# Performance work log

Hardware: AMD Instinct MI355X
Metric: run time of the kernel (lower is better)

The kernel has to match this reference:

```python
import jax, jax.numpy as jnp
import numpy as np

B, D = 128, 64  # batch; channel == height == width == dim == 64 (hardcoded by the module)


def setup_inputs() -> dict:
    key = jax.random.key(0)
    kx, kc, kh, kw = jax.random.split(key, 4)
    x = jax.random.normal(kx, (B, D, D, D), dtype=jnp.float32)
    # Stacked 1x1 conv weights: [i (loop index), out_channels, in_channels]
    Wc = jax.random.normal(kc, (D, D, D), dtype=jnp.float32) * 0.1
    Wh = jax.random.normal(kh, (D, D, D), dtype=jnp.float32) * 0.1
    Ww = jax.random.normal(kw, (D, D, D), dtype=jnp.float32) * 0.1
    return {"x": x, "Wc": Wc, "Wh": Wh, "Ww": Ww}


def reference(x, Wc, Wh, Ww):
    # x: [b, c, h, w] with c == h == w == 64
    # Adaptive avg-pool to 1x1 on three permutations -> three [b, 64] vectors.
    c_vec = x.mean(axis=(2, 3))  # pool over (h, w): channel descriptor   [b, 64]
    h_vec = x.mean(axis=(1, 2))  # pool over (c, h): width descriptor    [b, 64]
    w_vec = x.mean(axis=(1, 3))  # pool over (c, w): height descriptor   [b, 64]

    # All 64 per-iteration 1x1 convs + sigmoid as one batched GEMM per branch.
    # Wc[i, o, j]: weight of the i-th conv; conv(C)[o] = sum_j Wc[i,o,j] * c_vec[b,j]
    fc = jax.nn.sigmoid(jnp.einsum('ioj,bj->bio', Wc, c_vec))  # [b, 64(i), 64]
    fh = jax.nn.sigmoid(jnp.einsum('ioj,bj->bio', Wh, h_vec))  # [b, 64(i), 64]
    fw = jax.nn.sigmoid(jnp.einsum('ioj,bj->bio', Ww, w_vec))  # [b, 64(i), 64]

    # recon: bmm(bmm(C, H), W) == outer product fc_i (x) fh_i (x) fw_i, summed over i.
    LR = jnp.einsum('bic,bip,biq->bcpq', fc, fh, fw)  # [b, 64, 64, 64]
    return LR
```

## Files before the change

kernel.cpp:

```cpp
#include <hip/hip_runtime.h>
#include <hip/hip_bf16.h>


#define NB 128

typedef __attribute__((ext_vector_type(8))) short bf16x8;
typedef __attribute__((ext_vector_type(4))) float f32x4;

__device__ __forceinline__ float bf2f(short s) {
    return __uint_as_float(((unsigned)(unsigned short)s) << 16);
}
__device__ __forceinline__ unsigned packbf2(float a, float b) {
    unsigned ua = __float_as_uint(a); ua += 0x7fffu + ((ua >> 16) & 1u);
    unsigned ub = __float_as_uint(b); ub += 0x7fffu + ((ub >> 16) & 1u);
    return (ua >> 16) | (ub & 0xffff0000u);
}
__device__ __forceinline__ unsigned short f2bf(float f) {
    unsigned u = __float_as_uint(f); u += 0x7fffu + ((u >> 16) & 1u);
    return (unsigned short)(u >> 16);
}

__global__ __launch_bounds__(256) void pool_kernel(const float* __restrict__ x,
                                                   float* __restrict__ cvecT,
                                                   float* __restrict__ hv_part,
                                                   float* __restrict__ wv_part)
{
    const int blk  = blockIdx.x;
    const int b    = blk >> 3;
    const int cblk = blk & 7;
    const int t    = threadIdx.x;
    const int wv   = t >> 6;
    const int l    = t & 63;
    const int lg   = l >> 4;
    const int lw   = l & 15;

    __shared__ float cpart[8][4];
    __shared__ float hsum_l[64];
    __shared__ float wpart[4][64];

    const float* xb = x + (size_t)b * 262144 + (size_t)cblk * 32768;

    float cs[8];
    float acc_h[4] = {0.f, 0.f, 0.f, 0.f};
    float acc_w[4] = {0.f, 0.f, 0.f, 0.f};

#pragma unroll
    for (int cc = 0; cc < 8; ++cc) {
        const float* xc = xb + cc * 4096 + wv * 1024 + 4 * l;
        float sc = 0.f;
#pragma unroll
        for (int k = 0; k < 4; ++k) {
            float4 v = *reinterpret_cast<const float4*>(xc + k * 256);
            float s = (v.x + v.y) + (v.z + v.w);
            sc += s;
            acc_h[k] += s;
            acc_w[0] += v.x; acc_w[1] += v.y; acc_w[2] += v.z; acc_w[3] += v.w;
        }
        cs[cc] = sc;
    }

#pragma unroll
    for (int cc = 0; cc < 8; ++cc) {
        float v = cs[cc];
#pragma unroll
        for (int off = 32; off >= 1; off >>= 1) v += __shfl_xor(v, off, 64);
        if (l == 0) cpart[cc][wv] = v;
    }
#pragma unroll
    for (int k = 0; k < 4; ++k) {
        float v = acc_h[k];
        v += __shfl_xor(v, 1, 64);
        v += __shfl_xor(v, 2, 64);
        v += __shfl_xor(v, 4, 64);
        v += __shfl_xor(v, 8, 64);
        if (lw == 0) hsum_l[wv * 16 + k * 4 + lg] = v;
    }
#pragma unroll
    for (int m = 0; m < 4; ++m) {
        float v = acc_w[m];
        v += __shfl_xor(v, 16, 64);
        v += __shfl_xor(v, 32, 64);
        if (lg == 0) wpart[wv][lw * 4 + m] = v;
    }
    __syncthreads();

    const float scale = 1.f / 4096.f;
    if (t < 8) {
        float s = cpart[t][0] + cpart[t][1] + cpart[t][2] + cpart[t][3];
        cvecT[(cblk * 8 + t) * NB + b] = s * scale;
    }
    if (t < 64) {
        wv_part[(cblk * 64 + t) * NB + b] = hsum_l[t] * scale;
        float ws_ = wpart[0][t] + wpart[1][t] + wpart[2][t] + wpart[3][t];
        hv_part[(cblk * 64 + t) * NB + b] = ws_ * scale;
    }
}

__global__ __launch_bounds__(256) void fvec_kernel(const float* __restrict__ Wc,
                                                   const float* __restrict__ Wh,
                                                   const float* __restrict__ Ww,
                                                   const float* __restrict__ cvecT,
                                                   const float* __restrict__ hv_part,
                                                   const float* __restrict__ wv_part,
                                                   unsigned short* __restrict__ fcT,
                                                   unsigned short* __restrict__ fhT,
                                                   unsigned short* __restrict__ fwT)
{
    const int br = blockIdx.x >> 6;
    const int i  = blockIdx.x & 63;
    const float* W = (br == 0) ? Wc : (br == 1) ? Wh : Ww;
    const float* V = (br == 0) ? cvecT : (br == 1) ? hv_part : wv_part;
    unsigned short* outT = (br == 0) ? fcT : (br == 1) ? fhT : fwT;

    __shared__ float Wt[64][64];
    __shared__ float vl[64 * NB];

    const int t = threadIdx.x;
    {
        const float* Wi = W + (size_t)i * 4096;
#pragma unroll
        for (int r = 0; r < 4; ++r) {
            int f = t + 256 * r;
            float4 v = reinterpret_cast<const float4*>(Wi)[f];
            int o = (4 * f) >> 6;
            int j = (4 * f) & 63;
            Wt[j + 0][o] = v.x; Wt[j + 1][o] = v.y; Wt[j + 2][o] = v.z; Wt[j + 3][o] = v.w;
        }
    }
#pragma unroll
    for (int r = 0; r < 8; ++r) {
        int f = t + 256 * r;
        float4 v = reinterpret_cast<const float4*>(V)[f];
        if (br != 0) {
#pragma unroll
            for (int k = 1; k < 8; ++k) {
                float4 u = reinterpret_cast<const float4*>(V + 8192 * k)[f];
                v.x += u.x; v.y += u.y; v.z += u.z; v.w += u.w;
            }
        }
        reinterpret_cast<float4*>(vl)[f] = v;
    }
    __syncthreads();

    const int og = t & 7;
    const int bg = t >> 3;
    const int o0 = og * 8;
    const int b0 = bg * 4;

    float acc[4][8];
#pragma unroll
    for (int bb = 0; bb < 4; ++bb)
#pragma unroll
        for (int oo = 0; oo < 8; ++oo) acc[bb][oo] = 0.f;

#pragma unroll 4
    for (int j = 0; j < 64; ++j) {
        float4 vb = *reinterpret_cast<const float4*>(&vl[j * NB + b0]);
        float4 w0 = *reinterpret_cast<const float4*>(&Wt[j][o0]);
        float4 w1 = *reinterpret_cast<const float4*>(&Wt[j][o0 + 4]);
        float vb_[4] = {vb.x, vb.y, vb.z, vb.w};
        float wv_[8] = {w0.x, w0.y, w0.z, w0.w, w1.x, w1.y, w1.z, w1.w};
#pragma unroll
        for (int bb = 0; bb < 4; ++bb)
#pragma unroll
            for (int oo = 0; oo < 8; ++oo)
                acc[bb][oo] += vb_[bb] * wv_[oo];
    }

#pragma unroll
    for (int bb = 0; bb < 4; ++bb)
#pragma unroll
        for (int oo = 0; oo < 8; ++oo) {
            float sg = 1.f / (1.f + __expf(-acc[bb][oo]));
            outT[((size_t)(b0 + bb) * 64 + (o0 + oo)) * 64 + i] = f2bf(sg);
        }
}

__global__ __launch_bounds__(256) void recon_kernel(const unsigned short* __restrict__ fcT,
                                                    const unsigned short* __restrict__ fhT,
                                                    const unsigned short* __restrict__ fwT,
                                                    float* __restrict__ out)
{
    const int blk = blockIdx.x;
    const int b   = blk >> 2;
    const int cq  = blk & 3;
    const int t   = threadIdx.x;
    const int w   = t >> 6;
    const int l   = t & 63;
    const int lr  = l & 15;
    const int lg4 = l >> 4;

    __shared__ __align__(16) unsigned short fhl[64 * 72];
    __shared__ __align__(16) unsigned short fwl[64 * 72];
    __shared__ __align__(16) unsigned short fcl[16 * 72];

    const unsigned short* fhb = fhT + (size_t)b * 4096;
    const unsigned short* fwb = fwT + (size_t)b * 4096;
    const unsigned short* fcb = fcT + (size_t)b * 4096 + cq * 1024;

#pragma unroll
    for (int r = 0; r < 2; ++r) {
        int f = t + 256 * r;
        *reinterpret_cast<int4*>(&fhl[(f >> 3) * 72 + (f & 7) * 8]) =
            reinterpret_cast<const int4*>(fhb)[f];
        *reinterpret_cast<int4*>(&fwl[(f >> 3) * 72 + (f & 7) * 8]) =
            reinterpret_cast<const int4*>(fwb)[f];
    }
    if (t < 128) {
        *reinterpret_cast<int4*>(&fcl[(t >> 3) * 72 + (t & 7) * 8]) =
            reinterpret_cast<const int4*>(fcb)[t];
    }
    __syncthreads();

    bf16x8 afw[4][2];
#pragma unroll
    for (int qt = 0; qt < 4; ++qt)
#pragma unroll
        for (int kb = 0; kb < 2; ++kb)
            afw[qt][kb] = *reinterpret_cast<const bf16x8*>(
                &fwl[(qt * 16 + lr) * 72 + kb * 32 + lg4 * 8]);

    float hvf[4][2][8];
#pragma unroll
    for (int pt = 0; pt < 4; ++pt)
#pragma unroll
        for (int kb = 0; kb < 2; ++kb) {
            bf16x8 h = *reinterpret_cast<const bf16x8*>(
                &fhl[(pt * 16 + lr) * 72 + kb * 32 + lg4 * 8]);
#pragma unroll
            for (int j = 0; j < 8; ++j) hvf[pt][kb][j] = bf2f(h[j]);
        }

    for (int cc = 0; cc < 4; ++cc) {
        const int cl = w * 4 + cc;
        float cvf[16];
#pragma unroll
        for (int kb = 0; kb < 2; ++kb) {
            bf16x8 cf = *reinterpret_cast<const bf16x8*>(
                &fcl[cl * 72 + kb * 32 + lg4 * 8]);
#pragma unroll
            for (int j = 0; j < 8; ++j) cvf[kb * 8 + j] = bf2f(cf[j]);
        }
        bf16x8 bp[4][2];
#pragma unroll
        for (int pt = 0; pt < 4; ++pt)
#pragma unroll
            for (int kb = 0; kb < 2; ++kb) {
                union { unsigned u[4]; bf16x8 v; } bu;
#pragma unroll
                for (int jj = 0; jj < 4; ++jj) {
                    float p0 = cvf[kb * 8 + 2 * jj]     * hvf[pt][kb][2 * jj];
                    float p1 = cvf[kb * 8 + 2 * jj + 1] * hvf[pt][kb][2 * jj + 1];
                    bu.u[jj] = packbf2(p0, p1);
                }
                bp[pt][kb] = bu.v;
            }
        float* oc = out + (((size_t)b * 64 + cq * 16 + cl) * 64) * 64;
#pragma unroll
        for (int pt = 0; pt < 4; ++pt)
#pragma unroll
            for (int qt = 0; qt < 4; ++qt) {
                f32x4 a = {0.f, 0.f, 0.f, 0.f};
                a = __builtin_amdgcn_mfma_f32_16x16x32_bf16(afw[qt][0], bp[pt][0], a, 0, 0, 0);
                a = __builtin_amdgcn_mfma_f32_16x16x32_bf16(afw[qt][1], bp[pt][1], a, 0, 0, 0);
                float4 v; v.x = a[0]; v.y = a[1]; v.z = a[2]; v.w = a[3];
                *reinterpret_cast<float4*>(
                    oc + ((size_t)(pt * 16 + lr) * 64) + qt * 16 + lg4 * 4) = v;
            }
    }
}

extern "C" void kernel_launch(void* const* d_in, const int* in_sizes, int n_in,
                              void* d_out, int out_size, void* d_ws, size_t ws_size,
                              hipStream_t stream) {
    (void)in_sizes; (void)n_in; (void)out_size; (void)ws_size;
    const float* x  = (const float*)d_in[0];
    const float* Wc = (const float*)d_in[1];
    const float* Wh = (const float*)d_in[2];
    const float* Ww = (const float*)d_in[3];
    float* out = (float*)d_out;

    float* ws      = (float*)d_ws;
    float* cvecT   = ws;
    float* hv_part = ws + 8192;
    float* wv_part = ws + 73728;
    unsigned short* fcT = (unsigned short*)(ws + 139264);
    unsigned short* fhT = fcT + 524288;
    unsigned short* fwT = fhT + 524288;

    pool_kernel<<<1024, 256, 0, stream>>>(x, cvecT, hv_part, wv_part);
    fvec_kernel<<<192, 256, 0, stream>>>(Wc, Wh, Ww, cvecT, hv_part, wv_part, fcT, fhT, fwT);
    recon_kernel<<<512, 256, 0, stream>>>(fcT, fhT, fwT, out);
}
```

Baseline: 70.98 us.

## Fuse pool, fvec and recon kernels into one persistent kernel with grid barriers

Merges the three launches into a single 512-block kernel that uses atomic-counter grid barriers between the pooling, gate-GEMM and reconstruction phases. This removes two kernel launch gaps. The pool phase now covers 16 channels per block, so there are 4 partial slices instead of 8 to sum. It relies on all 512 blocks being co-resident (launch_bounds 256,2 and 48KB of shared memory), adds a memset launch, and risks deadlock or barrier spin overhead if occupancy is insufficient.

```diff
diff --git a/kernel.cpp b/kernel.cpp
--- a/kernel.cpp
+++ b/kernel.cpp
@@ -20,253 +20,268 @@
     return (unsigned short)(u >> 16);
 }
 
-__global__ __launch_bounds__(256) void pool_kernel(const float* __restrict__ x,
-                                                   float* __restrict__ cvecT,
-                                                   float* __restrict__ hv_part,
-                                                   float* __restrict__ wv_part)
-{
-    const int blk  = blockIdx.x;
-    const int b    = blk >> 3;
-    const int cblk = blk & 7;
-    const int t    = threadIdx.x;
-    const int wv   = t >> 6;
-    const int l    = t & 63;
-    const int lg   = l >> 4;
-    const int lw   = l & 15;
-
-    __shared__ float cpart[8][4];
-    __shared__ float hsum_l[64];
-    __shared__ float wpart[4][64];
-
-    const float* xb = x + (size_t)b * 262144 + (size_t)cblk * 32768;
-
-    float cs[8];
-    float acc_h[4] = {0.f, 0.f, 0.f, 0.f};
-    float acc_w[4] = {0.f, 0.f, 0.f, 0.f};
-
-#pragma unroll
-    for (int cc = 0; cc < 8; ++cc) {
-        const float* xc = xb + cc * 4096 + wv * 1024 + 4 * l;
-        float sc = 0.f;
-#pragma unroll
-        for (int k = 0; k < 4; ++k) {
-            float4 v = *reinterpret_cast<const float4*>(xc + k * 256);
-            float s = (v.x + v.y) + (v.z + v.w);
-            sc += s;
-            acc_h[k] += s;
-            acc_w[0] += v.x; acc_w[1] += v.y; acc_w[2] += v.z; acc_w[3] += v.w;
-        }
-        cs[cc] = sc;
-    }
-
-#pragma unroll
-    for (int cc = 0; cc < 8; ++cc) {
-        float v = cs[cc];
-#pragma unroll
-        for (int off = 32; off >= 1; off >>= 1) v += __shfl_xor(v, off, 64);
-        if (l == 0) cpart[cc][wv] = v;
-    }
-#pragma unroll
-    for (int k = 0; k < 4; ++k) {
-        float v = acc_h[k];
-        v += __shfl_xor(v, 1, 64);
-        v += __shfl_xor(v, 2, 64);
-        v += __shfl_xor(v, 4, 64);
-        v += __shfl_xor(v, 8, 64);
-        if (lw == 0) hsum_l[wv * 16 + k * 4 + lg] = v;
-    }
-#pragma unroll
-    for (int m = 0; m < 4; ++m) {
-        float v = acc_w[m];
-        v += __shfl_xor(v, 16, 64);
-        v += __shfl_xor(v, 32, 64);
-        if (lg == 0) wpart[wv][lw * 4 + m] = v;
+__device__ __forceinline__ void grid_barrier(unsigned* cnt, unsigned target) {
+    __syncthreads();
+    if (threadIdx.x == 0) {
+        __threadfence();
+        atomicAdd(cnt, 1u);
+        while (__hip_atomic_load(cnt, __ATOMIC_RELAXED,
+                                 __HIP_MEMORY_SCOPE_AGENT) < target) {
+            __builtin_amdgcn_s_sleep(2);
+        }
+        __threadfence();
     }
     __syncthreads();
-
-    const float scale = 1.f / 4096.f;
-    if (t < 8) {
-        float s = cpart[t][0] + cpart[t][1] + cpart[t][2] + cpart[t][3];
-        cvecT[(cblk * 8 + t) * NB + b] = s * scale;
+}
+
+__global__ __launch_bounds__(256, 2) void fused_kernel(
+    const float* __restrict__ x,
+    const float* __restrict__ Wc,
+    const float* __restrict__ Wh,
+    const float* __restrict__ Ww,
+    float* __restrict__ cvecT,
+    float* __restrict__ hv_part,
+    float* __restrict__ wv_part,
+    unsigned short* __restrict__ fcT,
+    unsigned short* __restrict__ fhT,
+    unsigned short* __restrict__ fwT,
+    unsigned* __restrict__ bar,
+    float* __restrict__ out)
+{
+    __shared__ __align__(16) unsigned char smem_raw[49152];
+    const int t = threadIdx.x;
+
+    {
+        float* cpart  = (float*)smem_raw;
+        float* hsum_l = cpart + 64;
+        float* wpart  = hsum_l + 64;
+
+        const int blk  = blockIdx.x;
+        const int b    = blk >> 2;
+        const int cblk = blk & 3;
+        const int wvv  = t >> 6;
+        const int l    = t & 63;
+        const int lg   = l >> 4;
+        const int lw   = l & 15;
+
+        const float* xb = x + (size_t)b * 262144 + (size_t)cblk * 65536;
+
+        float cs[16];
+        float acc_h[4] = {0.f, 0.f, 0.f, 0.f};
+        float acc_w[4] = {0.f, 0.f, 0.f, 0.f};
+
+#pragma unroll
+        for (int cc = 0; cc < 16; ++cc) {
+            const float* xc = xb + cc * 4096 + wvv * 1024 + 4 * l;
+            float sc = 0.f;
+#pragma unroll
+            for (int k = 0; k < 4; ++k) {
+                float4 v = *reinterpret_cast<const float4*>(xc + k * 256);
+                float s = (v.x + v.y) + (v.z + v.w);
+                sc += s;
+                acc_h[k] += s;
+                acc_w[0] += v.x; acc_w[1] += v.y; acc_w[2] += v.z; acc_w[3] += v.w;
+            }
+            cs[cc] = sc;
+        }
+
+#pragma unroll
+        for (int cc = 0; cc < 16; ++cc) {
+            float v = cs[cc];
+#pragma unroll
+            for (int off = 32; off >= 1; off >>= 1) v += __shfl_xor(v, off, 64);
+            if (l == 0) cpart[cc * 4 + wvv] = v;
+        }
+#pragma unroll
+        for (int k = 0; k < 4; ++k) {
+            float v = acc_h[k];
+            v += __shfl_xor(v, 1, 64);
+            v += __shfl_xor(v, 2, 64);
+            v += __shfl_xor(v, 4, 64);
+            v += __shfl_xor(v, 8, 64);
+            if (lw == 0) hsum_l[wvv * 16 + k * 4 + lg] = v;
+        }
+#pragma unroll
+        for (int m = 0; m < 4; ++m) {
+            float v = acc_w[m];
+            v += __shfl_xor(v, 16, 64);
+            v += __shfl_xor(v, 32, 64);
+            if (lg == 0) wpart[wvv * 64 + lw * 4 + m] = v;
+        }
+        __syncthreads();
+
+        const float scale = 1.f / 4096.f;
+        if (t < 16) {
+            float s = cpart[t * 4 + 0] + cpart[t * 4 + 1] + cpart[t * 4 + 2] + cpart[t * 4 + 3];
+            cvecT[(cblk * 16 + t) * NB + b] = s * scale;
+        }
+        if (t < 64) {
+            wv_part[(cblk * 64 + t) * NB + b] = hsum_l[t] * scale;
+            float ws_ = wpart[0 * 64 + t] + wpart[1 * 64 + t] + wpart[2 * 64 + t] + wpart[3 * 64 + t];
+            hv_part[(cblk * 64 + t) * NB + b] = ws_ * scale;
+        }
     }
-    if (t < 64) {
-        wv_part[(cblk * 64 + t) * NB + b] = hsum_l[t] * scale;
-        float ws_ = wpart[0][t] + wpart[1][t] + wpart[2][t] + wpart[3][t];
-        hv_part[(cblk * 64 + t) * NB + b] = ws_ * scale;
+    grid_barrier(&bar[0], 512);
+
+    if (blockIdx.x < 192) {
+        float* Wt = (float*)smem_raw;
+        float* vl = Wt + 4096;
+
+        const int br = blockIdx.x >> 6;
+        const int i  = blockIdx.x & 63;
+        const float* W = (br == 0) ? Wc : (br == 1) ? Wh : Ww;
+        const float* V = (br == 0) ? cvecT : (br == 1) ? hv_part : wv_part;
+        unsigned short* outT = (br == 0) ? fcT : (br == 1) ? fhT : fwT;
+
+        {
+            const float* Wi = W + (size_t)i * 4096;
+#pragma unroll
+            for (int r = 0; r < 4; ++r) {
+                int f = t + 256 * r;
+                float4 v = reinterpret_cast<const float4*>(Wi)[f];
+                int o = (4 * f) >> 6;
+                int j = (4 * f) & 63;
+                Wt[(j + 0) * 64 + o] = v.x; Wt[(j + 1) * 64 + o] = v.y;
+                Wt[(j + 2) * 64 + o] = v.z; Wt[(j + 3) * 64 + o] = v.w;
+            }
+        }
+#pragma unroll
+        for (int r = 0; r < 8; ++r) {
+            int f = t + 256 * r;
+            float4 v = reinterpret_cast<const float4*>(V)[f];
+            if (br != 0) {
+#pragma unroll
+                for (int k = 1; k < 4; ++k) {
+                    float4 u = reinterpret_cast<const float4*>(V + 8192 * k)[f];
+                    v.x += u.x; v.y += u.y; v.z += u.z; v.w += u.w;
+                }
+            }
+            reinterpret_cast<float4*>(vl)[f] = v;
+        }
+        __syncthreads();
+
+        const int og = t & 7;
+        const int bg = t >> 3;
+        const int o0 = og * 8;
+        const int b0 = bg * 4;
+
+        float acc[4][8];
+#pragma unroll
+        for (int bb = 0; bb < 4; ++bb)
+#pragma unroll
+            for (int oo = 0; oo < 8; ++oo) acc[bb][oo] = 0.f;
+
+#pragma unroll 4
+        for (int j = 0; j < 64; ++j) {
+            float4 vb = *reinterpret_cast<const float4*>(&vl[j * NB + b0]);
+            float4 w0 = *reinterpret_cast<const float4*>(&Wt[j * 64 + o0]);
+            float4 w1 = *reinterpret_cast<const float4*>(&Wt[j * 64 + o0 + 4]);
+            float vb_[4] = {vb.x, vb.y, vb.z, vb.w};
+            float wv_[8] = {w0.x, w0.y, w0.z, w0.w, w1.x, w1.y, w1.z, w1.w};
+#pragma unroll
+            for (int bb = 0; bb < 4; ++bb)
+#pragma unroll
+                for (int oo = 0; oo < 8; ++oo)
+                    acc[bb][oo] += vb_[bb] * wv_[oo];
+        }
+
+#pragma unroll
+        for (int bb = 0; bb < 4; ++bb)
+#pragma unroll
+            for (int oo = 0; oo < 8; ++oo) {
+                float sg = 1.f / (1.f + __expf(-acc[bb][oo]));
+                outT[((size_t)(b0 + bb) * 64 + (o0 + oo)) * 64 + i] = f2bf(sg);
+            }
     }
-}
-
-__global__ __launch_bounds__(256) void fvec_kernel(const float* __restrict__ Wc,
-                                                   const float* __restrict__ Wh,
-                                                   const float* __restrict__ Ww,
-                                                   const float* __restrict__ cvecT,
-                                                   const float* __restrict__ hv_part,
-                                                   const float* __restrict__ wv_part,
-                                                   unsigned short* __restrict__ fcT,
-                                                   unsigned short* __restrict__ fhT,
-                                                   unsigned short* __restrict__ fwT)
-{
-    const int br = blockIdx.x >> 6;
-    const int i  = blockIdx.x & 63;
-    const float* W = (br == 0) ? Wc : (br == 1) ? Wh : Ww;
-    const float* V = (br == 0) ? cvecT : (br == 1) ? hv_part : wv_part;
-    unsigned short* outT = (br == 0) ? fcT : (br == 1) ? fhT : fwT;
-
-    __shared__ float Wt[64][64];
-    __shared__ float vl[64 * NB];
-
-    const int t = threadIdx.x;
+    grid_barrier(&bar[1], 512);
+
     {
-        const float* Wi = W + (size_t)i * 4096;
-#pragma unroll
-        for (int r = 0; r < 4; ++r) {
+        unsigned short* fhl = (unsigned short*)smem_raw;
+        unsigned short* fwl = fhl + 64 * 72;
+        unsigned short* fcl = fwl + 64 * 72;
+
+        const int blk = blockIdx.x;
+        const int b   = blk >> 2;
+        const int cq  = blk & 3;
+        const int w   = t >> 6;
+        const int l   = t & 63;
+        const int lr  = l & 15;
+        const int lg4 = l >> 4;
+
+        const unsigned short* fhb = fhT + (size_t)b * 4096;
+        const unsigned short* fwb = fwT + (size_t)b * 4096;
+        const unsigned short* fcb = fcT + (size_t)b * 4096 + cq * 1024;
+
+#pragma unroll
+        for (int r = 0; r < 2; ++r) {
             int f = t + 256 * r;
-            float4 v = reinterpret_cast<const float4*>(Wi)[f];
-            int o = (4 * f) >> 6;
-            int j = (4 * f) & 63;
-            Wt[j + 0][o] = v.x; Wt[j + 1][o] = v.y; Wt[j + 2][o] = v.z; Wt[j + 3][o] = v.w;
-        }
-    }
-#pragma unroll
-    for (int r = 0; r < 8; ++r) {
-        int f = t + 256 * r;
-        float4 v = reinterpret_cast<const float4*>(V)[f];
-        if (br != 0) {
-#pragma unroll
-            for (int k = 1; k < 8; ++k) {
-                float4 u = reinterpret_cast<const float4*>(V + 8192 * k)[f];
-                v.x += u.x; v.y += u.y; v.z += u.z; v.w += u.w;
-            }
-        }
-        reinterpret_cast<float4*>(vl)[f] = v;
-    }
-    __syncthreads();
-
-    const int og = t & 7;
-    const int bg = t >> 3;
-    const int o0 = og * 8;
-    const int b0 = bg * 4;
-
-    float acc[4][8];
-#pragma unroll
-    for (int bb = 0; bb < 4; ++bb)
-#pragma unroll
-        for (int oo = 0; oo < 8; ++oo) acc[bb][oo] = 0.f;
-
-#pragma unroll 4
-    for (int j = 0; j < 64; ++j) {
-        float4 vb = *reinterpret_cast<const float4*>(&vl[j * NB + b0]);
-        float4 w0 = *reinterpret_cast<const float4*>(&Wt[j][o0]);
-        float4 w1 = *reinterpret_cast<const float4*>(&Wt[j][o0 + 4]);
-        float vb_[4] = {vb.x, vb.y, vb.z, vb.w};
-        float wv_[8] = {w0.x, w0.y, w0.z, w0.w, w1.x, w1.y, w1.z, w1.w};
-#pragma unroll
-        for (int bb = 0; bb < 4; ++bb)
-#pragma unroll
-            for (int oo = 0; oo < 8; ++oo)
-                acc[bb][oo] += vb_[bb] * wv_[oo];
-    }
-
-#pragma unroll
-    for (int bb = 0; bb < 4; ++bb)
-#pragma unroll
-        for (int oo = 0; oo < 8; ++oo) {
-            float sg = 1.f / (1.f + __expf(-acc[bb][oo]));
-            outT[((size_t)(b0 + bb) * 64 + (o0 + oo)) * 64 + i] = f2bf(sg);
-        }
-}
-
-__global__ __launch_bounds__(256) void recon_kernel(const unsigned short* __restrict__ fcT,
-                                                    const unsigned short* __restrict__ fhT,
-                                                    const unsigned short* __restrict__ fwT,
-                                                    float* __restrict__ out)
-{
-    const int blk = blockIdx.x;
-    const int b   = blk >> 2;
-    const int cq  = blk & 3;
-    const int t   = threadIdx.x;
-    const int w   = t >> 6;
-    const int l   = t & 63;
-    const int lr  = l & 15;
-    const int lg4 = l >> 4;
-
-    __shared__ __align__(16) unsigned short fhl[64 * 72];
-    __shared__ __align__(16) unsigned short fwl[64 * 72];
-    __shared__ __align__(16) unsigned short fcl[16 * 72];
-
-    const unsigned short* fhb = fhT + (size_t)b * 4096;
-    const unsigned short* fwb = fwT + (size_t)b * 4096;
-    const unsigned short* fcb = fcT + (size_t)b * 4096 + cq * 1024;
-
-#pragma unroll
-    for (int r = 0; r < 2; ++r) {
-        int f = t + 256 * r;
-        *reinterpret_cast<int4*>(&fhl[(f >> 3) * 72 + (f & 7) * 8]) =
-            reinterpret_cast<const int4*>(fhb)[f];
-        *reinterpret_cast<int4*>(&fwl[(f >> 3) * 72 + (f & 7) * 8]) =
-            reinterpret_cast<const int4*>(fwb)[f];
-    }
-    if (t < 128) {
-        *reinterpret_cast<int4*>(&fcl[(t >> 3) * 72 + (t & 7) * 8]) =
-            reinterpret_cast<const int4*>(fcb)[t];
-    }
-    __syncthreads();
-
-    bf16x8 afw[4][2];
-#pragma unroll
-    for (int qt = 0; qt < 4; ++qt)
-#pragma unroll
-        for (int kb = 0; kb < 2; ++kb)
-            afw[qt][kb] = *reinterpret_cast<const bf16x8*>(
-                &fwl[(qt * 16 + lr) * 72 + kb * 32 + lg4 * 8]);
-
-    float hvf[4][2][8];
-#pragma unroll
-    for (int pt = 0; pt < 4; ++pt)
-#pragma unroll
-        for (int kb = 0; kb < 2; ++kb) {
-            bf16x8 h = *reinterpret_cast<const bf16x8*>(
-                &fhl[(pt * 16 + lr) * 72 + kb * 32 + lg4 * 8]);
-#pragma unroll
-            for (int j = 0; j < 8; ++j) hvf[pt][kb][j] = bf2f(h[j]);
-        }
-
-    for (int cc = 0; cc < 4; ++cc) {
-        const int cl = w * 4 + cc;
-        float cvf[16];
-#pragma unroll
-        for (int kb = 0; kb < 2; ++kb) {
-            bf16x8 cf = *reinterpret_cast<const bf16x8*>(
-                &fcl[cl * 72 + kb * 32 + lg4 * 8]);
-#pragma unroll
-            for (int j = 0; j < 8; ++j) cvf[kb * 8 + j] = bf2f(cf[j]);
-        }
-        bf16x8 bp[4][2];
+            *reinterpret_cast<int4*>(&fhl[(f >> 3) * 72 + (f & 7) * 8]) =
+                reinterpret_cast<const int4*>(fhb)[f];
+            *reinterpret_cast<int4*>(&fwl[(f >> 3) * 72 + (f & 7) * 8]) =
+                reinterpret_cast<const int4*>(fwb)[f];
+        }
+        if (t < 128) {
+            *reinterpret_cast<int4*>(&fcl[(t >> 3) * 72 + (t & 7) * 8]) =
+                reinterpret_cast<const int4*>(fcb)[t];
+        }
+        __syncthreads();
+
+        bf16x8 afw[4][2];
+#pragma unroll
+        for (int qt = 0; qt < 4; ++qt)
+#pragma unroll
+            for (int kb = 0; kb < 2; ++kb)
+                afw[qt][kb] = *reinterpret_cast<const bf16x8*>(
+                    &fwl[(qt * 16 + lr) * 72 + kb * 32 + lg4 * 8]);
+
+        float hvf[4][2][8];
 #pragma unroll
         for (int pt = 0; pt < 4; ++pt)
 #pragma unroll
             for (int kb = 0; kb < 2; ++kb) {
-                union { unsigned u[4]; bf16x8 v; } bu;
-#pragma unroll
-                for (int jj = 0; jj < 4; ++jj) {
-                    float p0 = cvf[kb * 8 + 2 * jj]     * hvf[pt][kb][2 * jj];
-                    float p1 = cvf[kb * 8 + 2 * jj + 1] * hvf[pt][kb][2 * jj + 1];
-                    bu.u[jj] = packbf2(p0, p1);
+                bf16x8 h = *reinterpret_cast<const bf16x8*>(
+                    &fhl[(pt * 16 + lr) * 72 + kb * 32 + lg4 * 8]);
+#pragma unroll
+                for (int j = 0; j < 8; ++j) hvf[pt][kb][j] = bf2f(h[j]);
+            }
+
+        for (int cc = 0; cc < 4; ++cc) {
+            const int cl = w * 4 + cc;
+            float cvf[16];
+#pragma unroll
+            for (int kb = 0; kb < 2; ++kb) {
+                bf16x8 cf = *reinterpret_cast<const bf16x8*>(
+                    &fcl[cl * 72 + kb * 32 + lg4 * 8]);
+#pragma unroll
+                for (int j = 0; j < 8; ++j) cvf[kb * 8 + j] = bf2f(cf[j]);
+            }
+            bf16x8 bp[4][2];
+#pragma unroll
+            for (int pt = 0; pt < 4; ++pt)
+#pragma unroll
+                for (int kb = 0; kb < 2; ++kb) {
+                    union { unsigned u[4]; bf16x8 v; } bu;
+#pragma unroll
+                    for (int jj = 0; jj < 4; ++jj) {
+                        float p0 = cvf[kb * 8 + 2 * jj]     * hvf[pt][kb][2 * jj];
+                        float p1 = cvf[kb * 8 + 2 * jj + 1] * hvf[pt][kb][2 * jj + 1];
+                        bu.u[jj] = packbf2(p0, p1);
+                    }
+                    bp[pt][kb] = bu.v;
                 }
-                bp[pt][kb] = bu.v;
-            }
-        float* oc = out + (((size_t)b * 64 + cq * 16 + cl) * 64) * 64;
-#pragma unroll
-        for (int pt = 0; pt < 4; ++pt)
-#pragma unroll
-            for (int qt = 0; qt < 4; ++qt) {
-                f32x4 a = {0.f, 0.f, 0.f, 0.f};
-                a = __builtin_amdgcn_mfma_f32_16x16x32_bf16(afw[qt][0], bp[pt][0], a, 0, 0, 0);
-                a = __builtin_amdgcn_mfma_f32_16x16x32_bf16(afw[qt][1], bp[pt][1], a, 0, 0, 0);
-                float4 v; v.x = a[0]; v.y = a[1]; v.z = a[2]; v.w = a[3];
-                *reinterpret_cast<float4*>(
-                    oc + ((size_t)(pt * 16 + lr) * 64) + qt * 16 + lg4 * 4) = v;
-            }
+            float* oc = out + (((size_t)b * 64 + cq * 16 + cl) * 64) * 64;
+#pragma unroll
+            for (int pt = 0; pt < 4; ++pt)
+#pragma unroll
+                for (int qt = 0; qt < 4; ++qt) {
+                    f32x4 a = {0.f, 0.f, 0.f, 0.f};
+                    a = __builtin_amdgcn_mfma_f32_16x16x32_bf16(afw[qt][0], bp[pt][0], a, 0, 0, 0);
+                    a = __builtin_amdgcn_mfma_f32_16x16x32_bf16(afw[qt][1], bp[pt][1], a, 0, 0, 0);
+                    float4 v; v.x = a[0]; v.y = a[1]; v.z = a[2]; v.w = a[3];
+                    *reinterpret_cast<float4*>(
+                        oc + ((size_t)(pt * 16 + lr) * 64) + qt * 16 + lg4 * 4) = v;
+                }
+        }
     }
 }
 
@@ -283,12 +298,13 @@
     float* ws      = (float*)d_ws;
     float* cvecT   = ws;
     float* hv_part = ws + 8192;
-    float* wv_part = ws + 73728;
-    unsigned short* fcT = (unsigned short*)(ws + 139264);
+    float* wv_part = ws + 40960;
+    unsigned short* fcT = (unsigned short*)(ws + 73728);
     unsigned short* fhT = fcT + 524288;
     unsigned short* fwT = fhT + 524288;
-
-    pool_kernel<<<1024, 256, 0, stream>>>(x, cvecT, hv_part, wv_part);
-    fvec_kernel<<<192, 256, 0, stream>>>(Wc, Wh, Ww, cvecT, hv_part, wv_part, fcT, fhT, fwT);
-    recon_kernel<<<512, 256, 0, stream>>>(fcT, fhT, fwT, out);
-}
+    unsigned* bar = (unsigned*)(ws + 73728 + 786432);
+
+    hipMemsetAsync(bar, 0, 2 * sizeof(unsigned), stream);
+    fused_kernel<<<512, 256, 0, stream>>>(x, Wc, Wh, Ww, cvecT, hv_part, wv_part,
+                                          fcT, fhT, fwT, bar, out);
+}
```

Measured after the change: 239.0 us. 3.37x slower.
